# Optimization experiments

Measured on AMD Instinct MI355X. Metric: run time of the kernel, lower is better.

## Reference

```python
import jax, jax.numpy as jnp
import numpy as np

NUM_SEGMENTS = 64
HIDDEN = 1024
RANK = 16
N = 8192


def _xavier(key, shape):
    fan_in, fan_out = shape[-2], shape[-1]
    limit = (6.0 / (fan_in + fan_out)) ** 0.5
    return jax.random.uniform(key, shape, jnp.float32, -limit, limit)


def setup_inputs() -> dict:
    key = jax.random.key(0)
    k1, k2, k3, k4 = jax.random.split(key, 4)
    return {
        "math_hidden_states": jax.random.normal(k1, (N, HIDDEN), jnp.float32),
        "segment_ids": jax.random.randint(k2, (N,), 0, NUM_SEGMENTS, jnp.int64),
        "A_matrices": _xavier(k3, (NUM_SEGMENTS, HIDDEN, RANK)),
        "B_matrices": _xavier(k4, (NUM_SEGMENTS, RANK, HIDDEN)),
        "bias": jnp.zeros((NUM_SEGMENTS, HIDDEN), jnp.float32),
    }


def reference(math_hidden_states, segment_ids, A_matrices, B_matrices, bias):
    # gather per-token low-rank factors: A [N,H,R], B [N,R,H]
    gathered_A = A_matrices[segment_ids]
    gathered_B = B_matrices[segment_ids]
    # intermediate = B @ x  -> [N, R]
    intermediate = jnp.einsum('nrh,nh->nr', gathered_B, math_hidden_states)
    # transformed = A @ intermediate -> [N, H]
    transformed = jnp.einsum('nhr,nr->nh', gathered_A, intermediate)
    return transformed + bias[segment_ids]
```

## Files before the change

kernel.cpp:

```cpp
#include <hip/hip_runtime.h>

#define HID 1024
#define RANK 16
#define NSEG 64
#define NXCD 8


__global__ __launch_bounds__(1024) void k1_hist(
    const int* __restrict__ seg, int N,
    int* __restrict__ base_c, int* __restrict__ cursor,
    int* __restrict__ sorted, int slots)
{
    __shared__ int hist[NSEG];
    __shared__ int pbase[NSEG];
    __shared__ int paddedTotal;
    const int tid = threadIdx.x;
    if (tid < NSEG) hist[tid] = 0;
    __syncthreads();
    for (int i = tid; i < N; i += 1024) atomicAdd(&hist[seg[i]], 1);
    __syncthreads();
    if (tid == 0) {
        int run = 0;
        for (int s = 0; s < NSEG; ++s) { pbase[s] = run; run += (hist[s] + 3) & ~3; }
        paddedTotal = run;
    }
    __syncthreads();
    if (tid < NSEG) {
        base_c[tid] = pbase[tid];
        cursor[tid] = 0;
        const int c0 = hist[tid], c1 = (hist[tid] + 3) & ~3;
        for (int k = c0; k < c1; ++k) sorted[pbase[tid] + k] = -1;
    }
    for (int i = paddedTotal + tid; i < slots; i += 1024) sorted[i] = -1;
}

__global__ __launch_bounds__(256) void k2_scatter(
    const int* __restrict__ seg, int N,
    const int* __restrict__ base_c, int* __restrict__ cursor,
    int* __restrict__ sorted)
{
    const int i = blockIdx.x * 256 + threadIdx.x;
    if (i < N) {
        const int s = seg[i];
        const int pos = atomicAdd(&cursor[s], 1);
        sorted[base_c[s] + pos] = (s << 14) | i;
    }
}

__global__ __launch_bounds__(256) void lora_apply(
    const float* __restrict__ x,
    const int*   __restrict__ sorted,
    const float* __restrict__ A,
    const float* __restrict__ B,
    const float* __restrict__ bias,
    float*       __restrict__ out,
    int tilesPerXcd)
{
    const int work = (blockIdx.x & (NXCD - 1)) * tilesPerXcd + (blockIdx.x >> 3);
    const int tid  = threadIdx.x;
    const int lane = tid & 63;
    const int wave = tid >> 6;

    __shared__ float red[4][16][68];
    __shared__ float inter_lds[4][RANK];

    int e[4];
    #pragma unroll
    for (int j = 0; j < 4; ++j) e[j] = sorted[work * 4 + j];
    if (e[0] < 0) return;
    const int s = e[0] >> 14;

    int  n[4];
    bool valid[4];
    #pragma unroll
    for (int j = 0; j < 4; ++j) {
        valid[j] = e[j] >= 0;
        n[j] = (valid[j] ? e[j] : e[0]) & 16383;
    }

    const float4* A4 = (const float4*)(A + (size_t)s * HID * RANK);
    float4 av[4][4];
    #pragma unroll
    for (int jh = 0; jh < 4; ++jh)
        #pragma unroll
        for (int q = 0; q < 4; ++q)
            av[jh][q] = A4[(size_t)(tid * 4 + jh) * (RANK / 4) + q];
    const float4 bia = ((const float4*)(bias + (size_t)s * HID))[tid];

    float4 xv[4][4];
    #pragma unroll
    for (int j = 0; j < 4; ++j) {
        const float4* xr = (const float4*)(x + (size_t)n[j] * HID);
        #pragma unroll
        for (int k = 0; k < 4; ++k) xv[j][k] = xr[k * 64 + lane];
    }

    const float4* B4 = (const float4*)(B + (size_t)s * RANK * HID);
    float acc[4][4];
    #pragma unroll
    for (int rr = 0; rr < 4; ++rr)
        #pragma unroll
        for (int j = 0; j < 4; ++j) acc[rr][j] = 0.f;

    #pragma unroll
    for (int rr = 0; rr < 4; ++rr) {
        const float4* Br = B4 + (size_t)(wave * 4 + rr) * (HID / 4);
        #pragma unroll
        for (int k = 0; k < 4; ++k) {
            float4 b = Br[k * 64 + lane];
            #pragma unroll
            for (int j = 0; j < 4; ++j)
                acc[rr][j] += b.x * xv[j][k].x + b.y * xv[j][k].y
                            + b.z * xv[j][k].z + b.w * xv[j][k].w;
        }
    }

    #pragma unroll
    for (int rr = 0; rr < 4; ++rr)
        #pragma unroll
        for (int j = 0; j < 4; ++j)
            red[wave][rr * 4 + j][lane] = acc[rr][j];

    const int v = lane & 15;
    const int q = lane >> 4;
    const float4* rp = (const float4*)&red[wave][v][q * 16];
    float4 r0 = rp[0], r1 = rp[1], r2 = rp[2], r3 = rp[3];
    float sum = ((r0.x + r0.y) + (r0.z + r0.w))
              + ((r1.x + r1.y) + (r1.z + r1.w))
              + ((r2.x + r2.y) + (r2.z + r2.w))
              + ((r3.x + r3.y) + (r3.z + r3.w));
    sum += __shfl_xor(sum, 16, 64);
    sum += __shfl_xor(sum, 32, 64);
    if (lane < 16) inter_lds[v & 3][wave * 4 + (v >> 2)] = sum;
    __syncthreads();

    #pragma unroll
    for (int j = 0; j < 4; ++j) {
        const float4* I4 = (const float4*)inter_lds[j];
        float4 iv[4];
        #pragma unroll
        for (int qq = 0; qq < 4; ++qq) iv[qq] = I4[qq];
        float4 o = bia;
        float* op = (float*)&o;
        #pragma unroll
        for (int jh = 0; jh < 4; ++jh) {
            float a = 0.f;
            #pragma unroll
            for (int qq = 0; qq < 4; ++qq)
                a += av[jh][qq].x * iv[qq].x + av[jh][qq].y * iv[qq].y
                   + av[jh][qq].z * iv[qq].z + av[jh][qq].w * iv[qq].w;
            op[jh] += a;
        }
        if (valid[j])
            ((float4*)(out + (size_t)n[j] * HID))[tid] = o;
    }
}

extern "C" void kernel_launch(void* const* d_in, const int* in_sizes, int n_in,
                              void* d_out, int out_size, void* d_ws, size_t ws_size,
                              hipStream_t stream) {
    const float* x    = (const float*)d_in[0];
    const int*   seg  = (const int*)d_in[1];
    const float* A    = (const float*)d_in[2];
    const float* B    = (const float*)d_in[3];
    const float* bias = (const float*)d_in[4];
    float* out = (float*)d_out;

    const int N = in_sizes[1];

    int tiles = ((N + 3) / 4 + NSEG + 7) & ~7;
    const int slots = tiles * 4;

    int* wsi    = (int*)d_ws;
    int* base_c = wsi;
    int* cursor = wsi + NSEG;
    int* sorted = wsi + 2 * NSEG;

    k1_hist   <<<1, 1024, 0, stream>>>(seg, N, base_c, cursor, sorted, slots);
    k2_scatter<<<(N + 255) / 256, 256, 0, stream>>>(seg, N, base_c, cursor, sorted);
    lora_apply<<<tiles, 256, 0, stream>>>(x, sorted, A, B, bias, out, tiles / NXCD);
}
```

Baseline: 137.8 us.

## Group 16 tokens per block with tile descriptors and LDS-staged activations

Raises the number of same-segment tokens handled per workgroup from 4 to 16. Activations are staged in LDS and each B row is loaded once per tile, with the reduction done in four passes. A parallel prefix scan builds per-tile descriptors holding segment, count and start. The goal is to cut repeated B/A loads and the block count, at the cost of more padding waste per segment, more LDS and registers per block, and fewer blocks to hide latency.

```diff
diff --git a/kernel.cpp b/kernel.cpp
--- a/kernel.cpp
+++ b/kernel.cpp
@@ -3,139 +3,158 @@
 #define HID 1024
 #define RANK 16
 #define NSEG 64
+#define G 16
 #define NXCD 8
 
 
-__global__ __launch_bounds__(1024) void k1_hist(
+__global__ __launch_bounds__(1024) void k_hist_scan(
     const int* __restrict__ seg, int N,
-    int* __restrict__ base_c, int* __restrict__ cursor,
-    int* __restrict__ sorted, int slots)
+    int* __restrict__ base_g, int* __restrict__ cursor_g,
+    int* __restrict__ desc_g, int gtiles)
 {
     __shared__ int hist[NSEG];
-    __shared__ int pbase[NSEG];
-    __shared__ int paddedTotal;
+    __shared__ int ltot;
     const int tid = threadIdx.x;
     if (tid < NSEG) hist[tid] = 0;
     __syncthreads();
     for (int i = tid; i < N; i += 1024) atomicAdd(&hist[seg[i]], 1);
     __syncthreads();
-    if (tid == 0) {
-        int run = 0;
-        for (int s = 0; s < NSEG; ++s) { pbase[s] = run; run += (hist[s] + 3) & ~3; }
-        paddedTotal = run;
-    }
-    __syncthreads();
-    if (tid < NSEG) {
-        base_c[tid] = pbase[tid];
-        cursor[tid] = 0;
-        const int c0 = hist[tid], c1 = (hist[tid] + 3) & ~3;
-        for (int k = c0; k < c1; ++k) sorted[pbase[tid] + k] = -1;
-    }
-    for (int i = paddedTotal + tid; i < slots; i += 1024) sorted[i] = -1;
-}
-
-__global__ __launch_bounds__(256) void k2_scatter(
+
+    if (tid < 64) {
+        const int h = hist[tid];
+        const int p = (h + 15) & ~15;
+        int v = p;
+        #pragma unroll
+        for (int off = 1; off < 64; off <<= 1) {
+            int u = __shfl_up(v, off, 64);
+            if (tid >= off) v += u;
+        }
+        const int b = v - p;
+        base_g[tid]   = b;
+        cursor_g[tid] = 0;
+        if (tid == 63) ltot = v;
+        const int nt = (h + 15) >> 4;
+        for (int k = 0; k < nt; ++k) {
+            const int cnt = min(16, h - (k << 4));
+            desc_g[(b >> 4) + k] = (tid << 19) | (cnt << 14) | (b + (k << 4));
+        }
+    }
+    __syncthreads();
+    const int totTiles = ltot >> 4;
+    for (int t = totTiles + tid; t < gtiles; t += 1024) desc_g[t] = -1;
+}
+
+__global__ __launch_bounds__(256) void k_scatter(
     const int* __restrict__ seg, int N,
-    const int* __restrict__ base_c, int* __restrict__ cursor,
+    const int* __restrict__ base_g, int* __restrict__ cursor_g,
     int* __restrict__ sorted)
 {
     const int i = blockIdx.x * 256 + threadIdx.x;
     if (i < N) {
         const int s = seg[i];
-        const int pos = atomicAdd(&cursor[s], 1);
-        sorted[base_c[s] + pos] = (s << 14) | i;
-    }
-}
-
-__global__ __launch_bounds__(256) void lora_apply(
+        const int pos = atomicAdd(&cursor_g[s], 1);
+        sorted[base_g[s] + pos] = i;
+    }
+}
+
+__global__ __launch_bounds__(256) void k_apply(
     const float* __restrict__ x,
     const int*   __restrict__ sorted,
+    const int*   __restrict__ desc,
     const float* __restrict__ A,
     const float* __restrict__ B,
     const float* __restrict__ bias,
     float*       __restrict__ out,
-    int tilesPerXcd)
+    int chunkPerXcd)
 {
-    const int work = (blockIdx.x & (NXCD - 1)) * tilesPerXcd + (blockIdx.x >> 3);
+    const int work = (blockIdx.x & (NXCD - 1)) * chunkPerXcd + (blockIdx.x >> 3);
+    const int d = desc[work];
+    if (d < 0) return;
+    const int s     = d >> 19;
+    const int cnt   = (d >> 14) & 31;
+    const int start = d & 16383;
+
     const int tid  = threadIdx.x;
     const int lane = tid & 63;
-    const int wave = tid >> 6;
-
-    __shared__ float red[4][16][68];
-    __shared__ float inter_lds[4][RANK];
-
-    int e[4];
-    #pragma unroll
-    for (int j = 0; j < 4; ++j) e[j] = sorted[work * 4 + j];
-    if (e[0] < 0) return;
-    const int s = e[0] >> 14;
-
-    int  n[4];
-    bool valid[4];
-    #pragma unroll
-    for (int j = 0; j < 4; ++j) {
-        valid[j] = e[j] >= 0;
-        n[j] = (valid[j] ? e[j] : e[0]) & 16383;
-    }
+    const int w    = tid >> 6;
+
+    __shared__ float4 x_lds[G][HID / 4];
+    __shared__ float  red[4][16][68];
+    __shared__ float  inter_lds[G][RANK];
+
+    const int n0 = sorted[start];
+
+    #pragma unroll
+    for (int jj = 0; jj < 4; ++jj) {
+        const int j  = w * 4 + jj;
+        const int nj = (j < cnt) ? sorted[start + j] : n0;
+        const float4* xr = (const float4*)(x + (size_t)nj * HID);
+        #pragma unroll
+        for (int k = 0; k < 4; ++k)
+            x_lds[j][k * 64 + lane] = xr[k * 64 + lane];
+    }
+
+    int n[G];
+    #pragma unroll
+    for (int j = 0; j < G; ++j)
+        n[j] = (j < cnt) ? sorted[start + j] : n0;
+
+    __syncthreads();
+
+    const float4* B4 = (const float4*)(B + (size_t)s * RANK * HID);
+    float acc[4][G];
+    #pragma unroll
+    for (int rr = 0; rr < 4; ++rr)
+        #pragma unroll
+        for (int j = 0; j < G; ++j) acc[rr][j] = 0.f;
+
+    #pragma unroll
+    for (int k = 0; k < 4; ++k) {
+        float4 b[4];
+        #pragma unroll
+        for (int rr = 0; rr < 4; ++rr)
+            b[rr] = B4[(size_t)(w * 4 + rr) * (HID / 4) + k * 64 + lane];
+        #pragma unroll
+        for (int j = 0; j < G; ++j) {
+            const float4 xj = x_lds[j][k * 64 + lane];
+            #pragma unroll
+            for (int rr = 0; rr < 4; ++rr)
+                acc[rr][j] += b[rr].x * xj.x + b[rr].y * xj.y
+                            + b[rr].z * xj.z + b[rr].w * xj.w;
+        }
+    }
+
+    const int v = lane & 15;
+    const int q = lane >> 4;
+    #pragma unroll
+    for (int p = 0; p < 4; ++p) {
+        #pragma unroll
+        for (int idx = 0; idx < 16; ++idx)
+            red[w][idx][lane] = acc[idx >> 2][p * 4 + (idx & 3)];
+        const float4* rp = (const float4*)&red[w][v][q * 16];
+        float4 r0 = rp[0], r1 = rp[1], r2 = rp[2], r3 = rp[3];
+        float sum = ((r0.x + r0.y) + (r0.z + r0.w))
+                  + ((r1.x + r1.y) + (r1.z + r1.w))
+                  + ((r2.x + r2.y) + (r2.z + r2.w))
+                  + ((r3.x + r3.y) + (r3.z + r3.w));
+        sum += __shfl_xor(sum, 16, 64);
+        sum += __shfl_xor(sum, 32, 64);
+        if (lane < 16)
+            inter_lds[p * 4 + (v & 3)][w * 4 + (v >> 2)] = sum;
+    }
+    __syncthreads();
 
     const float4* A4 = (const float4*)(A + (size_t)s * HID * RANK);
     float4 av[4][4];
     #pragma unroll
     for (int jh = 0; jh < 4; ++jh)
         #pragma unroll
-        for (int q = 0; q < 4; ++q)
-            av[jh][q] = A4[(size_t)(tid * 4 + jh) * (RANK / 4) + q];
+        for (int qq = 0; qq < 4; ++qq)
+            av[jh][qq] = A4[(size_t)(tid * 4 + jh) * (RANK / 4) + qq];
     const float4 bia = ((const float4*)(bias + (size_t)s * HID))[tid];
 
-    float4 xv[4][4];
-    #pragma unroll
-    for (int j = 0; j < 4; ++j) {
-        const float4* xr = (const float4*)(x + (size_t)n[j] * HID);
-        #pragma unroll
-        for (int k = 0; k < 4; ++k) xv[j][k] = xr[k * 64 + lane];
-    }
-
-    const float4* B4 = (const float4*)(B + (size_t)s * RANK * HID);
-    float acc[4][4];
-    #pragma unroll
-    for (int rr = 0; rr < 4; ++rr)
-        #pragma unroll
-        for (int j = 0; j < 4; ++j) acc[rr][j] = 0.f;
-
-    #pragma unroll
-    for (int rr = 0; rr < 4; ++rr) {
-        const float4* Br = B4 + (size_t)(wave * 4 + rr) * (HID / 4);
-        #pragma unroll
-        for (int k = 0; k < 4; ++k) {
-            float4 b = Br[k * 64 + lane];
-            #pragma unroll
-            for (int j = 0; j < 4; ++j)
-                acc[rr][j] += b.x * xv[j][k].x + b.y * xv[j][k].y
-                            + b.z * xv[j][k].z + b.w * xv[j][k].w;
-        }
-    }
-
-    #pragma unroll
-    for (int rr = 0; rr < 4; ++rr)
-        #pragma unroll
-        for (int j = 0; j < 4; ++j)
-            red[wave][rr * 4 + j][lane] = acc[rr][j];
-
-    const int v = lane & 15;
-    const int q = lane >> 4;
-    const float4* rp = (const float4*)&red[wave][v][q * 16];
-    float4 r0 = rp[0], r1 = rp[1], r2 = rp[2], r3 = rp[3];
-    float sum = ((r0.x + r0.y) + (r0.z + r0.w))
-              + ((r1.x + r1.y) + (r1.z + r1.w))
-              + ((r2.x + r2.y) + (r2.z + r2.w))
-              + ((r3.x + r3.y) + (r3.z + r3.w));
-    sum += __shfl_xor(sum, 16, 64);
-    sum += __shfl_xor(sum, 32, 64);
-    if (lane < 16) inter_lds[v & 3][wave * 4 + (v >> 2)] = sum;
-    __syncthreads();
-
-    #pragma unroll
-    for (int j = 0; j < 4; ++j) {
+    #pragma unroll
+    for (int j = 0; j < G; ++j) {
         const float4* I4 = (const float4*)inter_lds[j];
         float4 iv[4];
         #pragma unroll
@@ -151,7 +170,7 @@
                    + av[jh][qq].z * iv[qq].z + av[jh][qq].w * iv[qq].w;
             op[jh] += a;
         }
-        if (valid[j])
+        if (j < cnt)
             ((float4*)(out + (size_t)n[j] * HID))[tid] = o;
     }
 }
@@ -167,16 +186,16 @@
     float* out = (float*)d_out;
 
     const int N = in_sizes[1];
-
-    int tiles = ((N + 3) / 4 + NSEG + 7) & ~7;
-    const int slots = tiles * 4;
+    const int gtiles = (((N + G - 1) / G) + NSEG + 7) & ~7;
 
     int* wsi    = (int*)d_ws;
-    int* base_c = wsi;
+    int* base_g = wsi;
     int* cursor = wsi + NSEG;
-    int* sorted = wsi + 2 * NSEG;
-
-    k1_hist   <<<1, 1024, 0, stream>>>(seg, N, base_c, cursor, sorted, slots);
-    k2_scatter<<<(N + 255) / 256, 256, 0, stream>>>(seg, N, base_c, cursor, sorted);
-    lora_apply<<<tiles, 256, 0, stream>>>(x, sorted, A, B, bias, out, tiles / NXCD);
-}
+    int* desc   = wsi + 2 * NSEG;
+    int* sorted = wsi + 2 * NSEG + gtiles;
+
+    k_hist_scan<<<1, 1024, 0, stream>>>(seg, N, base_g, cursor, desc, gtiles);
+    k_scatter  <<<(N + 255) / 256, 256, 0, stream>>>(seg, N, base_g, cursor, sorted);
+    k_apply    <<<gtiles, 256, 0, stream>>>(x, sorted, desc, A, B, bias, out,
+                                            gtiles / NXCD);
+}
```

Result: slower. 143.0 us (+3.8%).
